# Kernel optimization log

Hardware: AMD Instinct MI355X
Metric: run time of the kernel (lower is better)

## Reference

```python
import jax, jax.numpy as jnp
import numpy as np


def setup_inputs() -> dict:
    key = jax.random.key(0)
    k0, k1, k2, k3 = jax.random.split(key, 4)
    N, D, DEG, B = 20000, 128, 32, 1024
    features = jax.random.normal(k0, (N, D), jnp.float32)
    neighbors = jax.random.randint(k1, (N, DEG), 0, N, dtype=jnp.int32)
    train_index = jax.random.randint(k2, (B,), 0, N, dtype=jnp.int32)
    W = jax.random.normal(k3, (1, 2 * D), jnp.float32) * (1.0 / np.sqrt(2 * D))
    b = jnp.zeros((1,), jnp.float32)
    return {"features": features, "W": W, "b": b, "neighbors": neighbors,
            "train_index": train_index, "walk_times": 8, "batch_size": B}


def reference(features, W, b, neighbors, train_index, walk_times, batch_size):
    N, D = features.shape
    B = train_index.shape[0]
    rows = jnp.arange(B)[:, None]                       # [B,1]
    self_oh = jax.nn.one_hot(train_index, N, dtype=jnp.float32)  # [B,N]

    # Dense adjacency rows of the start nodes (== adj_sparse[batch] densified)
    nb0 = neighbors[train_index]                        # [B,deg]
    adj0 = jnp.zeros((B, N), jnp.float32).at[rows, nb0].set(1.0)

    chosen = self_oh                                    # visited mask (start node marked)
    candi_mask = (adj0 - chosen) > 0.0                  # non-self candidates

    # Per-edge learned score: relu(Linear(concat(f_x, f_y))) == relu(fx@Wx + fy@Wy + b)
    Wx, Wy = W[0, :D], W[0, D:]
    sx = features[train_index] @ Wx                     # [B]
    sy = features[nb0] @ Wy                             # [B,deg]
    s = jax.nn.relu(sx[:, None] + sy + b[0])            # [B,deg]
    scored = jnp.zeros((B, N), jnp.float32).at[rows, nb0].set(s)
    candi = jnp.where(candi_mask, scored, 0.0)
    # rows with no (or all-zero-scored) candidates fall back to a self-loop of weight 1
    candi = jnp.where((candi.sum(axis=1) == 0.0)[:, None], self_oh, candi)

    keys = jax.random.split(jax.random.key(42), walk_times)

    def step(carry, k):
        candi, chosen = carry
        # degenerate rows: resample the start node (safe fallback for empty support)
        p = jnp.where((candi.sum(axis=1) == 0.0)[:, None], self_oh, candi)
        # multinomial(p, 1) via Gumbel-max (categorical with probs proportional to p)
        logp = jnp.where(p > 0.0, jnp.log(jnp.where(p > 0.0, p, 1.0)), -jnp.inf)
        g = jax.random.gumbel(k, (p.shape[0], p.shape[1]), jnp.float32)
        new = jnp.argmax(logp + g, axis=1)              # [B]
        chosen = jnp.maximum(chosen, jax.nn.one_hot(new, p.shape[1], dtype=jnp.float32))
        adj_new = jnp.zeros_like(candi).at[rows, neighbors[new]].set(1.0)
        candi = ((candi - chosen + adj_new) > 0.0).astype(jnp.float32)
        return (candi, chosen), new

    (_, _), steps = jax.lax.scan(step, (candi, chosen), keys)  # steps: [T,B]
    walks = jnp.concatenate(
        [train_index[:, None].astype(jnp.int32), steps.T.astype(jnp.int32)], axis=1)
    return walks
```

## Files before the change

### kernel.cpp

```cpp
#include <hip/hip_runtime.h>
#include <cstdint>

namespace {

constexpr int N    = 20000;
constexpr int D    = 128;
constexpr int DEG  = 32;
constexpr int BB   = 1024;
constexpr int T    = 8;
constexpr int NC   = (N + 15) / 16;
constexpr int MAXC = 384;

__device__ __forceinline__ uint32_t rotl32(uint32_t x, int n) {
  return (x << n) | (x >> (32 - n));
}

__device__ __forceinline__ void threefry2x32(uint32_t k0, uint32_t k1,
                                             uint32_t x0, uint32_t x1,
                                             uint32_t& o0, uint32_t& o1) {
  const uint32_t ks2 = k0 ^ k1 ^ 0x1BD11BDAu;
  x0 += k0; x1 += k1;
#define TF_ROUND(r) { x0 += x1; x1 = rotl32(x1, (r)); x1 ^= x0; }
  TF_ROUND(13) TF_ROUND(15) TF_ROUND(26) TF_ROUND(6)
  x0 += k1;  x1 += ks2 + 1u;
  TF_ROUND(17) TF_ROUND(29) TF_ROUND(16) TF_ROUND(24)
  x0 += ks2; x1 += k0 + 2u;
  TF_ROUND(13) TF_ROUND(15) TF_ROUND(26) TF_ROUND(6)
  x0 += k0;  x1 += k1 + 3u;
  TF_ROUND(17) TF_ROUND(29) TF_ROUND(16) TF_ROUND(24)
  x0 += k1;  x1 += ks2 + 4u;
  TF_ROUND(13) TF_ROUND(15) TF_ROUND(26) TF_ROUND(6)
  x0 += ks2; x1 += k0 + 5u;
#undef TF_ROUND
  o0 = x0; o1 = x1;
}

__device__ __forceinline__ uint32_t rbits(uint32_t k0, uint32_t k1, uint32_t j) {
  uint32_t o0, o1;
  threefry2x32(k0, k1, 0u, j, o0, o1);
  return o0 ^ o1;
}

__device__ __forceinline__ float gumbel_f32(uint32_t bits) {
  const uint32_t mant = bits >> 9;
  const float u = (mant == 0u) ? 1.17549435e-38f
                               : (__uint_as_float(0x3F800000u | mant) - 1.0f);
  const float inner = -(float)log((double)u);
  return -(float)log((double)inner);
}

__device__ __forceinline__ uint32_t f2ord(float f) {
  const uint32_t b = __float_as_uint(f);
  return (b & 0x80000000u) ? ~b : (b | 0x80000000u);
}

template <int CTRL>
__device__ __forceinline__ uint32_t dppmov(uint32_t v) {
  return (uint32_t)__builtin_amdgcn_update_dpp((int)v, (int)v, CTRL, 0xF, 0xF, false);
}

__device__ __forceinline__ void wave_max64(uint32_t& hi, uint32_t& lo) {
#define RL(CTRL) { const uint32_t oh = dppmov<CTRL>(hi), ol = dppmov<CTRL>(lo); \
    if (oh > hi || (oh == hi && ol > lo)) { hi = oh; lo = ol; } }
  RL(0x111) RL(0x112) RL(0x114) RL(0x118) RL(0x142) RL(0x143)
#undef RL
  hi = (uint32_t)__builtin_amdgcn_readlane((int)hi, 63);
  lo = (uint32_t)__builtin_amdgcn_readlane((int)lo, 63);
}

__device__ __forceinline__ uint32_t cwd(int n)  { return (uint32_t)n >> 4; }
__device__ __forceinline__ uint32_t cbit(int n) { return 1u << (((uint32_t)n & 15u) << 1); }

__global__ __launch_bounds__(64)
void walk_kernel(const float* __restrict__ features,
                 const float* __restrict__ W,
                 const float* __restrict__ bptr,
                 const int*   __restrict__ neighbors,
                 const int*   __restrict__ train_index,
                 int* __restrict__ out)
{
  __shared__ uint32_t comb[NC];
  __shared__ int      lst[MAXC];
  __shared__ float    val0[DEG];

  const int lane = threadIdx.x;
  const int r    = blockIdx.x;
  const int self = train_index[r];
  const uint32_t rN = (uint32_t)(r * N);
  const uint64_t lower = (1ULL << lane) - 1ULL;

  int nbj = -1;
  if (lane < DEG) nbj = neighbors[(size_t)self * DEG + lane];

  {
    uint64_t* c8 = reinterpret_cast<uint64_t*>(comb);
    for (int i = lane; i < NC / 2; i += 64) c8[i] = 0ull;
  }

  uint32_t sk0, sk1;
  threefry2x32(0u, 42u, 0u, (uint32_t)lane, sk0, sk1);

  const float bval = bptr[0];
  const float* frow = features + (size_t)self * D;
  float acc = frow[lane] * W[lane] + frow[lane + 64] * W[lane + 64];
  for (int m = 1; m < 64; m <<= 1) acc += __shfl_xor(acc, m);
  const float sx = acc;

  float sval = 0.0f;
  if (lane < DEG) {
    const float* g  = features + (size_t)nbj * D;
    const float* wy = W + D;
    float a = 0.0f;
    for (int d = 0; d < D; d += 4) {
      const float4 f = *reinterpret_cast<const float4*>(g + d);
      const float4 w = *reinterpret_cast<const float4*>(wy + d);
      a += f.x * w.x; a += f.y * w.y; a += f.z * w.z; a += f.w * w.w;
    }
    sval = fmaxf((sx + a) + bval, 0.0f);
  }

  bool add0 = false;
  if (lane < DEG && nbj != self && sval > 0.0f) {
    const uint32_t old = atomicOr(&comb[cwd(nbj)], cbit(nbj));
    add0 = !(old & cbit(nbj));
  }
  const uint64_t m0 = __ballot(add0);
  if (add0) {
    const int p = (int)__popcll(m0 & lower);
    lst[p] = nbj; val0[p] = sval;
  }
  int cnt = (int)__popcll(m0);
  if (lane == 0) {
    atomicOr(&comb[cwd(self)], cbit(self) << 1);
    if (cnt == 0) {
      lst[0] = self; val0[0] = 1.0f;
      atomicOr(&comb[cwd(self)], cbit(self));
    }
  }
  if (cnt == 0) cnt = 1;

  int zom0 = 0, zom1 = 0, zom2 = 0, zom3 = 0, zmask = 0;
  uint32_t hiP = 0u, loP = 0u;

  for (int k = 0; k < T; ++k) {
    uint32_t hi, lo;
    if (k == 0) {
      const uint32_t kk0 = (uint32_t)__builtin_amdgcn_readlane((int)sk0, 0);
      const uint32_t kk1 = (uint32_t)__builtin_amdgcn_readlane((int)sk1, 0);
      hi = 0u; lo = 0u;
      if (lane < cnt) {
        const int c = lst[lane];
        const float v = (float)log((double)val0[lane])
                      + gumbel_f32(rbits(kk0, kk1, rN + (uint32_t)c));
        hi = f2ord(v); lo = ((0x7FFFFFu - (uint32_t)c) << 9) | (uint32_t)lane;
      }
    } else {
      hi = hiP; lo = loP;
    }
    wave_max64(hi, lo);
    const bool haveList = (cnt > 0);
    const int nn  = haveList ? (int)(0x7FFFFFu - (lo >> 9)) : self;
    const int pos = (int)(lo & 0x1FFu);

    if (lane == 0) out[r * (T + 1) + k + 1] = nn;
    if (k == T - 1) break;

    int nb = -1;
    if (lane < DEG) nb = neighbors[(size_t)nn * DEG + lane];

    if (lane == 0) atomicOr(&comb[cwd(nn)], cbit(nn) << 1);

    float v0f = 1.0f;
    if (k == 0 && haveList) v0f = val0[pos];

    if (haveList) {
      const int last = lst[cnt - 1];
      if (pos != cnt - 1 && lane == 0) lst[pos] = last;
      --cnt;
    }

    const uint32_t nk0 = (uint32_t)__builtin_amdgcn_readlane((int)sk0, k + 1);
    const uint32_t nk1 = (uint32_t)__builtin_amdgcn_readlane((int)sk1, k + 1);

    hiP = 0u; loP = 0u;
    for (int i = lane; i < cnt; i += 64) {
      const int c = lst[i];
      const uint32_t h = rbits(nk0, nk1, rN + (uint32_t)c) >> 9;
      const uint32_t l = ((0x7FFFFFu - (uint32_t)c) << 9) | (uint32_t)i;
      if (h > hiP || (h == hiP && l > loP)) { hiP = h; loP = l; }
    }

    const bool adNN = __any(nb == nn);
    const bool wasZ = ((zmask & 1) && zom0 == nn) || ((zmask & 2) && zom1 == nn) ||
                      ((zmask & 4) && zom2 == nn) || ((zmask & 8) && zom3 == nn);
    const bool stay = haveList &&
        ((k == 0) ? (((v0f - 1.0f) + (adNN ? 1.0f : 0.0f)) > 0.0f) : adNN);

    if (stay) {
      if (lane == 0) lst[cnt] = nn;
      const int posN = cnt; ++cnt;
      if (!wasZ) {
        if      (!(zmask & 1)) { zom0 = nn; zmask |= 1; }
        else if (!(zmask & 2)) { zom1 = nn; zmask |= 2; }
        else if (!(zmask & 4)) { zom2 = nn; zmask |= 4; }
        else                   { zom3 = nn; zmask |= 8; }
      }
      const uint32_t h = rbits(nk0, nk1, rN + (uint32_t)nn) >> 9;
      const uint32_t l = ((0x7FFFFFu - (uint32_t)nn) << 9) | (uint32_t)posN;
      if (h > hiP || (h == hiP && l > loP)) { hiP = h; loP = l; }
    } else if (wasZ) {
      if ((zmask & 1) && zom0 == nn) zmask &= ~1;
      else if ((zmask & 2) && zom1 == nn) zmask &= ~2;
      else if ((zmask & 4) && zom2 == nn) zmask &= ~4;
      else if ((zmask & 8) && zom3 == nn) zmask &= ~8;
    }

    bool zdrop = false;
    if (zmask) {
#define ZTEST(BIT, Z) \
      if ((zmask & BIT) && Z != nn) { \
        if (!__any(nb == Z)) { \
          int pz = -1; \
          for (int i = lane; i < cnt; i += 64) if (lst[i] == Z) pz = i; \
          const uint64_t fz = __ballot(pz >= 0); \
          const int sz = (int)(__ffsll((unsigned long long)fz) - 1); \
          pz = __shfl(pz, sz); \
          const int lastz = lst[cnt - 1]; \
          if (pz != cnt - 1 && lane == 0) lst[pz] = lastz; \
          --cnt; zmask &= ~BIT; zdrop = true; \
        } \
      }
      ZTEST(1, zom0) ZTEST(2, zom1) ZTEST(4, zom2) ZTEST(8, zom3)
#undef ZTEST
    }
    if (zdrop) {
      hiP = 0u; loP = 0u;
      for (int i = lane; i < cnt; i += 64) {
        const int c = lst[i];
        const uint32_t h = rbits(nk0, nk1, rN + (uint32_t)c) >> 9;
        const uint32_t l = ((0x7FFFFFu - (uint32_t)c) << 9) | (uint32_t)i;
        if (h > hiP || (h == hiP && l > loP)) { hiP = h; loP = l; }
      }
    }

    bool added = false;
    const int nbv = nb;
    if (lane < DEG) {
      const uint32_t old = atomicOr(&comb[cwd(nbv)], cbit(nbv));
      added = !(old & (cbit(nbv) | (cbit(nbv) << 1)));
    }
    const uint64_t ma = __ballot(added);
    const int mypos = cnt + (int)__popcll(ma & lower);
    if (added) {
      lst[mypos] = nbv;
      const uint32_t h = rbits(nk0, nk1, rN + (uint32_t)nbv) >> 9;
      const uint32_t l = ((0x7FFFFFu - (uint32_t)nbv) << 9) | (uint32_t)mypos;
      if (h > hiP || (h == hiP && l > loP)) { hiP = h; loP = l; }
    }
    cnt += (int)__popcll(ma);
  }
  if (lane == 0) out[r * (T + 1)] = self;
}

}

extern "C" void kernel_launch(void* const* d_in, const int* in_sizes, int n_in,
                              void* d_out, int out_size, void* d_ws, size_t ws_size,
                              hipStream_t stream) {
  const float* features  = (const float*)d_in[0];
  const float* W         = (const float*)d_in[1];
  const float* b         = (const float*)d_in[2];
  const int*   neighbors = (const int*)d_in[3];
  const int*   tindex    = (const int*)d_in[4];
  int* out = (int*)d_out;

  hipLaunchKernelGGL(walk_kernel, dim3(BB), dim3(64), 0, stream,
                     features, W, b, neighbors, tindex, out);
}
```

Measured before the change: 23.47 us.

## Speculatively prefetch likely next node's neighbors from surviving-candidate max

```diff
diff --git a/kernel.cpp b/kernel.cpp
--- a/kernel.cpp
+++ b/kernel.cpp
@@ -140,7 +140,9 @@
   if (cnt == 0) cnt = 1;
 
   int zom0 = 0, zom1 = 0, zom2 = 0, zom3 = 0, zmask = 0;
-  uint32_t hiP = 0u, loP = 0u;
+  uint32_t survH = 0u, survL = 0u;
+  uint32_t hiA = 0u, loA = 0u;
+  int prefId = -1, nbPre = -1;
 
   for (int k = 0; k < T; ++k) {
     uint32_t hi, lo;
@@ -154,11 +156,13 @@
                       + gumbel_f32(rbits(kk0, kk1, rN + (uint32_t)c));
         hi = f2ord(v); lo = ((0x7FFFFFu - (uint32_t)c) << 9) | (uint32_t)lane;
       }
+      wave_max64(hi, lo);
     } else {
-      hi = hiP; lo = loP;
-    }
-    wave_max64(hi, lo);
-    const bool haveList = (cnt > 0);
+      hi = hiA; lo = loA;
+      wave_max64(hi, lo);
+      if (survH > hi || (survH == hi && survL > lo)) { hi = survH; lo = survL; }
+    }
+    const bool haveList = (lo != 0u);
     const int nn  = haveList ? (int)(0x7FFFFFu - (lo >> 9)) : self;
     const int pos = (int)(lo & 0x1FFu);
 
@@ -166,28 +170,43 @@
     if (k == T - 1) break;
 
     int nb = -1;
-    if (lane < DEG) nb = neighbors[(size_t)nn * DEG + lane];
+    if (nn == prefId) {
+      nb = nbPre;
+    } else if (lane < DEG) {
+      nb = neighbors[(size_t)nn * DEG + lane];
+    }
 
     if (lane == 0) atomicOr(&comb[cwd(nn)], cbit(nn) << 1);
 
     float v0f = 1.0f;
     if (k == 0 && haveList) v0f = val0[pos];
+    int last = 0;
+    if (haveList) last = lst[cnt - 1];
+
+    const uint32_t nk0 = (uint32_t)__builtin_amdgcn_readlane((int)sk0, k + 1);
+    const uint32_t nk1 = (uint32_t)__builtin_amdgcn_readlane((int)sk1, k + 1);
+
+    uint32_t hiS = 0u, loS = 0u;
+    for (int i = lane; i < cnt; i += 64) {
+      if (i == pos) continue;
+      const int c = lst[i];
+      const uint32_t h = rbits(nk0, nk1, rN + (uint32_t)c) >> 9;
+      const uint32_t pay = (i == cnt - 1) ? (uint32_t)pos : (uint32_t)i;
+      const uint32_t l = ((0x7FFFFFu - (uint32_t)c) << 9) | pay;
+      if (h > hiS || (h == hiS && l > loS)) { hiS = h; loS = l; }
+    }
+    wave_max64(hiS, loS);
+    survH = hiS; survL = loS;
+
+    prefId = -1; nbPre = -1;
+    if (k < T - 2 && survL != 0u) {
+      prefId = (int)(0x7FFFFFu - (survL >> 9));
+      if (lane < DEG) nbPre = neighbors[(size_t)prefId * DEG + lane];
+    }
 
     if (haveList) {
-      const int last = lst[cnt - 1];
       if (pos != cnt - 1 && lane == 0) lst[pos] = last;
       --cnt;
-    }
-
-    const uint32_t nk0 = (uint32_t)__builtin_amdgcn_readlane((int)sk0, k + 1);
-    const uint32_t nk1 = (uint32_t)__builtin_amdgcn_readlane((int)sk1, k + 1);
-
-    hiP = 0u; loP = 0u;
-    for (int i = lane; i < cnt; i += 64) {
-      const int c = lst[i];
-      const uint32_t h = rbits(nk0, nk1, rN + (uint32_t)c) >> 9;
-      const uint32_t l = ((0x7FFFFFu - (uint32_t)c) << 9) | (uint32_t)i;
-      if (h > hiP || (h == hiP && l > loP)) { hiP = h; loP = l; }
     }
 
     const bool adNN = __any(nb == nn);
@@ -196,6 +215,7 @@
     const bool stay = haveList &&
         ((k == 0) ? (((v0f - 1.0f) + (adNN ? 1.0f : 0.0f)) > 0.0f) : adNN);
 
+    hiA = 0u; loA = 0u;
     if (stay) {
       if (lane == 0) lst[cnt] = nn;
       const int posN = cnt; ++cnt;
@@ -205,9 +225,8 @@
         else if (!(zmask & 4)) { zom2 = nn; zmask |= 4; }
         else                   { zom3 = nn; zmask |= 8; }
       }
-      const uint32_t h = rbits(nk0, nk1, rN + (uint32_t)nn) >> 9;
-      const uint32_t l = ((0x7FFFFFu - (uint32_t)nn) << 9) | (uint32_t)posN;
-      if (h > hiP || (h == hiP && l > loP)) { hiP = h; loP = l; }
+      hiA = rbits(nk0, nk1, rN + (uint32_t)nn) >> 9;
+      loA = ((0x7FFFFFu - (uint32_t)nn) << 9) | (uint32_t)posN;
     } else if (wasZ) {
       if ((zmask & 1) && zom0 == nn) zmask &= ~1;
       else if ((zmask & 2) && zom1 == nn) zmask &= ~2;
@@ -234,28 +253,31 @@
 #undef ZTEST
     }
     if (zdrop) {
-      hiP = 0u; loP = 0u;
+      uint32_t hR = 0u, lR = 0u;
       for (int i = lane; i < cnt; i += 64) {
         const int c = lst[i];
         const uint32_t h = rbits(nk0, nk1, rN + (uint32_t)c) >> 9;
         const uint32_t l = ((0x7FFFFFu - (uint32_t)c) << 9) | (uint32_t)i;
-        if (h > hiP || (h == hiP && l > loP)) { hiP = h; loP = l; }
+        if (h > hR || (h == hR && l > lR)) { hR = h; lR = l; }
       }
-    }
-
+      wave_max64(hR, lR);
+      survH = hR; survL = lR;
+      hiA = 0u; loA = 0u;
+    }
+
+    uint32_t hN = 0u;
+    if (lane < DEG) hN = rbits(nk0, nk1, rN + (uint32_t)nb) >> 9;
     bool added = false;
-    const int nbv = nb;
     if (lane < DEG) {
-      const uint32_t old = atomicOr(&comb[cwd(nbv)], cbit(nbv));
-      added = !(old & (cbit(nbv) | (cbit(nbv) << 1)));
+      const uint32_t old = atomicOr(&comb[cwd(nb)], cbit(nb));
+      added = !(old & (cbit(nb) | (cbit(nb) << 1)));
     }
     const uint64_t ma = __ballot(added);
     const int mypos = cnt + (int)__popcll(ma & lower);
     if (added) {
-      lst[mypos] = nbv;
-      const uint32_t h = rbits(nk0, nk1, rN + (uint32_t)nbv) >> 9;
-      const uint32_t l = ((0x7FFFFFu - (uint32_t)nbv) << 9) | (uint32_t)mypos;
-      if (h > hiP || (h == hiP && l > loP)) { hiP = h; loP = l; }
+      lst[mypos] = nb;
+      const uint32_t l = ((0x7FFFFFu - (uint32_t)nb) << 9) | (uint32_t)mypos;
+      if (hN > hiA || (hN == hiA && l > loA)) { hiA = hN; loA = l; }
     }
     cnt += (int)__popcll(ma);
   }
```

Measured after the change: 27.43 us. 1.17x slower.
